# Kernel optimization log

Hardware: AMD Instinct MI355X
Metric: run time of the kernel (lower is better)

## Reference

```python
import jax, jax.numpy as jnp
import numpy as np

H = 768
NH = 12
HD = H // NH
FF = 3072
EPS = 1e-12
SCALE = 1.0 / (HD ** 0.5)


def _ln(x, g, b):
    m = jnp.mean(x, axis=-1, keepdims=True)
    v = jnp.mean((x - m) ** 2, axis=-1, keepdims=True)
    return (x - m) * jax.lax.rsqrt(v + EPS) * g + b


def setup_inputs() -> dict:
    key = jax.random.key(0)
    ks = jax.random.split(key, 16)
    B, Q, S, T = 8, 64, 48, 128
    s = 0.02
    return {
        "q": jax.random.normal(ks[0], (B, Q, H), jnp.float32),
        "k": jax.random.normal(ks[1], (B, S, T, H), jnp.float32),
        "mask": jax.random.randint(ks[2], (B, S, T), 0, 2, jnp.int32),
        "Wq": jax.random.normal(ks[3], (H, H), jnp.float32) * s,
        "Wkv": jax.random.normal(ks[4], (H, H), jnp.float32) * s,
        "Wo": jax.random.normal(ks[5], (H, H), jnp.float32) * s,
        "bo": jnp.zeros((H,), jnp.float32),
        "ln1_g": jnp.ones((H,), jnp.float32),
        "ln1_b": jnp.zeros((H,), jnp.float32),
        "W1": jax.random.normal(ks[6], (H, FF), jnp.float32) * s,
        "b1": jnp.zeros((FF,), jnp.float32),
        "W2": jax.random.normal(ks[7], (FF, H), jnp.float32) * s,
        "b2": jnp.zeros((H,), jnp.float32),
        "ln2_g": jnp.ones((H,), jnp.float32),
        "ln2_b": jnp.zeros((H,), jnp.float32),
    }


def reference(q, k, mask, Wq, Wkv, Wo, bo, ln1_g, ln1_b, W1, b1, W2, b2, ln2_g, ln2_b):
    B, Q, _ = q.shape
    _, S, T, _ = k.shape
    # projections (no bias)
    qp = (q @ Wq).reshape(B, Q, NH, HD)            # [b,q,h,d]
    kv = (k @ Wkv).reshape(B, S, T, NH, HD)        # [b,s,t,h,d]
    # broadcast-query grouped attention: softmax only over token dim t
    scores = jnp.einsum('bqhd,bsthd->bhqst', qp, kv) * SCALE
    scores = scores + mask.astype(scores.dtype)[:, None, None, :, :] * -10000.0
    alpha = jax.nn.softmax(scores, axis=-1)        # dropout is identity in eval
    res = jnp.einsum('bhqst,bsthd->bqshd', alpha, kv).reshape(B, Q, S, H)
    # BertSelfOutput with zero residual (residual=False)
    attn_out = _ln(res @ Wo + bo, ln1_g, ln1_b)    # [b,q,s,H]
    # FFN
    ffn = jax.nn.gelu(attn_out @ W1 + b1, approximate=False) @ W2 + b2
    return _ln(attn_out + ffn, ln2_g, ln2_b)
```

## Files before the change

### kernel.cpp

```cpp
#include <hip/hip_runtime.h>
#include <hip/hip_bf16.h>
#include <math.h>

#define B_ 8
#define Q_ 64
#define S_ 48
#define T_ 128
#define H_ 768
#define NH_ 12
#define HD_ 64
#define FF_ 3072

typedef float f32x4 __attribute__((ext_vector_type(4)));
typedef short s16x8 __attribute__((ext_vector_type(8)));
typedef short s16x4 __attribute__((ext_vector_type(4)));

__device__ __forceinline__ float ldT(const float* p, size_t i) { return p[i]; }
__device__ __forceinline__ float ldT(const __hip_bfloat16* p, size_t i) { return __bfloat162float(p[i]); }
__device__ __forceinline__ void stT(float* p, size_t i, float v) { p[i] = v; }
__device__ __forceinline__ void stT(__hip_bfloat16* p, size_t i, float v) { p[i] = __float2bfloat16(v); }

__device__ __forceinline__ short f2bf(float f) {
  __hip_bfloat16 h = __float2bfloat16(f);
  return *reinterpret_cast<short*>(&h);
}

__device__ __forceinline__ float gelu_f(float x) {
  float z = 1.5957691216f * (x + 0.044715f * x * x * x);
  z = fminf(z, 80.0f);
  float e = __expf(z);
  return x * e / (e + 1.0f);
}

__device__ __forceinline__ void gld_lds16(const void* g, void* l) {
  __builtin_amdgcn_global_load_lds(
      (const __attribute__((address_space(1))) void*)g,
      (__attribute__((address_space(3))) void*)l, 16, 0, 0);
}

__device__ __forceinline__ int swz_off(int row, int kc) {
  return row * 64 + ((kc ^ ((row >> 1) & 3)) << 4);
}

#define WAITV4() asm volatile("s_waitcnt vmcnt(4)" ::: "memory")
#define WAITV5() asm volatile("s_waitcnt vmcnt(5)" ::: "memory")
#define WAITV0() asm volatile("s_waitcnt vmcnt(0)" ::: "memory")
#define BARX()   do { __builtin_amdgcn_s_barrier(); asm volatile("" ::: "memory"); } while (0)

template<int KK, typename OT, bool BIAS, bool GELU>
__global__ __launch_bounds__(256) void gemm_mfma(
    const __hip_bfloat16* __restrict__ A,
    const __hip_bfloat16* __restrict__ BT,
    const float* __restrict__ bias, OT* __restrict__ C,
    int N, int nbx, int GB)
{
  constexpr int NT = KK / 32;
  static_assert(NT % 3 == 0 && NT >= 6, "KK must be multiple of 96");
  __shared__ char sm[3][16384];

  const int cpx = gridDim.x >> 3;
  const int xcd = blockIdx.x & 7;
  const int ci  = blockIdx.x >> 3;
  const int gsz = GB * nbx;
  const int g   = ci / gsz;
  const int r2  = ci - g * gsz;
  const int bn  = r2 / GB;
  const int bi  = r2 - bn * GB;
  const int bm  = xcd * (cpx / nbx) + g * GB + bi;
  const int m0 = bm * 128, n0 = bn * 128;

  const int tid = threadIdx.x;
  const int lane = tid & 63;
  const int wid = tid >> 6;
  const int wr = wid >> 1, wc = wid & 1;
  const int kcg = lane >> 4, rl = lane & 15;

  const __hip_bfloat16* pA[2];
  const __hip_bfloat16* pB[2];
  #pragma unroll
  for (int r = 0; r < 2; ++r) {
    const int c = tid + r * 256, row = c >> 2, slot = c & 3;
    const int kc = slot ^ ((row >> 1) & 3);
    pA[r] = A + (size_t)(m0 + row) * KK + kc * 8;
    pB[r] = BT + (size_t)(n0 + row) * KK + kc * 8;
  }
  auto stageT = [&](char* base, int off) {
    gld_lds16(pA[0] + off, base + tid * 16);
    gld_lds16(pA[1] + off, base + tid * 16 + 4096);
    gld_lds16(pB[0] + off, base + 8192 + tid * 16);
    gld_lds16(pB[1] + off, base + 8192 + tid * 16 + 4096);
  };

  int woffA[4], woffB[4];
  #pragma unroll
  for (int m = 0; m < 4; ++m)
    woffA[m] = swz_off(wr * 64 + m * 16 + rl, kcg);
  #pragma unroll
  for (int n = 0; n < 4; ++n)
    woffB[n] = 8192 + swz_off(wc * 64 + n * 16 + rl, kcg);

  f32x4 acc[4][4] = {};
  s16x8 af[4], bf[4];
  auto reads = [&](const char* base) {
    #pragma unroll
    for (int m = 0; m < 4; ++m) af[m] = *(const s16x8*)(base + woffA[m]);
    #pragma unroll
    for (int n = 0; n < 4; ++n) bf[n] = *(const s16x8*)(base + woffB[n]);
  };
  auto mfmas = [&]() {
    #pragma unroll
    for (int m = 0; m < 4; ++m)
      #pragma unroll
      for (int n = 0; n < 4; ++n)
        acc[m][n] = __builtin_amdgcn_mfma_f32_16x16x32_bf16(af[m], bf[n], acc[m][n], 0, 0, 0);
  };

  stageT(sm[0], 0);
  stageT(sm[1], 32);
  #pragma unroll
  for (int r = 0; r < 2; ++r) { pA[r] += 64; pB[r] += 64; }

  #pragma unroll 1
  for (int it = 0; it < NT / 3 - 1; ++it) {
    WAITV4(); BARX(); reads(sm[0]); stageT(sm[2], 0);  mfmas();
    WAITV4(); BARX(); reads(sm[1]); stageT(sm[0], 32); mfmas();
    WAITV4(); BARX(); reads(sm[2]); stageT(sm[1], 64); mfmas();
    #pragma unroll
    for (int r = 0; r < 2; ++r) { pA[r] += 96; pB[r] += 96; }
  }
  WAITV4(); BARX(); reads(sm[0]); stageT(sm[2], 0); mfmas();
  WAITV4(); BARX(); reads(sm[1]); mfmas();
  WAITV0(); BARX(); reads(sm[2]); mfmas();

  const int colb = n0 + wc * 64 + rl;
  const int rowb = m0 + wr * 64 + (lane >> 4) * 4;
  float bv[4];
  #pragma unroll
  for (int n = 0; n < 4; ++n) bv[n] = BIAS ? bias[colb + n * 16] : 0.0f;
  #pragma unroll
  for (int m = 0; m < 4; ++m) {
    #pragma unroll
    for (int r = 0; r < 4; ++r) {
      const int row = rowb + m * 16 + r;
      #pragma unroll
      for (int n = 0; n < 4; ++n) {
        float v = acc[m][n][r] + bv[n];
        if (GELU) v = gelu_f(v);
        stT(C, (size_t)row * N + colb + n * 16, v);
      }
    }
  }
}

template<int KK, typename OT, bool BIAS, bool GELU>
__global__ __launch_bounds__(256, 2) void gemm_fat(
    const __hip_bfloat16* __restrict__ A,
    const __hip_bfloat16* __restrict__ BT,
    const float* __restrict__ bias, OT* __restrict__ C,
    int N, int nbx, int GB)
{
  constexpr int NT = KK / 32;
  static_assert(NT % 3 == 0 && NT >= 6, "KK must be multiple of 96");
  __shared__ char sm[3][20480];

  const int cpx = gridDim.x >> 3;
  const int xcd = blockIdx.x & 7;
  const int ci  = blockIdx.x >> 3;
  const int gsz = GB * nbx;
  const int g   = ci / gsz;
  const int r2  = ci - g * gsz;
  const int bn  = r2 / GB;
  const int bi  = r2 - bn * GB;
  const int bm  = xcd * (cpx / nbx) + g * GB + bi;
  const int m0 = bm * 128, n0 = bn * 192;

  const int tid = threadIdx.x;
  const int lane = tid & 63;
  const int wid = tid >> 6;
  const int wm = wid >> 1;
  const int wn = wid & 1;
  const int kcg = lane >> 4, rl = lane & 15;

  const __hip_bfloat16* pA[2];
  const __hip_bfloat16* pB[3];
  #pragma unroll
  for (int r = 0; r < 2; ++r) {
    const int c = tid + r * 256, row = c >> 2, slot = c & 3;
    const int kc = slot ^ ((row >> 1) & 3);
    pA[r] = A + (size_t)(m0 + row) * KK + kc * 8;
  }
  #pragma unroll
  for (int r = 0; r < 3; ++r) {
    const int c = tid + r * 256, row = c >> 2, slot = c & 3;
    const int kc = slot ^ ((row >> 1) & 3);
    pB[r] = BT + (size_t)(n0 + row) * KK + kc * 8;
  }
  auto stageT = [&](char* base, int off) {
    gld_lds16(pA[0] + off, base + tid * 16);
    gld_lds16(pA[1] + off, base + tid * 16 + 4096);
    gld_lds16(pB[0] + off, base + 8192 + tid * 16);
    gld_lds16(pB[1] + off, base + 8192 + tid * 16 + 4096);
    gld_lds16(pB[2] + off, base + 8192 + tid * 16 + 8192);
  };

  int woffA[4], woffB[6];
  #pragma unroll
  for (int m = 0; m < 4; ++m)
    woffA[m] = swz_off(wm * 64 + m * 16 + rl, kcg);
  #pragma unroll
  for (int n = 0; n < 6; ++n)
    woffB[n] = 8192 + swz_off(wn * 96 + n * 16 + rl, kcg);

  f32x4 acc[4][6] = {};
  s16x8 af[4], bf[6];
  auto reads = [&](const char* base) {
    #pragma unroll
    for (int m = 0; m < 4; ++m) af[m] = *(const s16x8*)(base + woffA[m]);
    #pragma unroll
    for (int n = 0; n < 6; ++n) bf[n] = *(const s16x8*)(base + woffB[n]);
  };
  auto mfmas = [&]() {
    #pragma unroll
    for (int m = 0; m < 4; ++m)
      #pragma unroll
      for (int n = 0; n < 6; ++n)
        acc[m][n] = __builtin_amdgcn_mfma_f32_16x16x32_bf16(af[m], bf[n], acc[m][n], 0, 0, 0);
  };

  stageT(sm[0], 0);
  stageT(sm[1], 32);
  #pragma unroll
  for (int r = 0; r < 2; ++r) pA[r] += 64;
  #pragma unroll
  for (int r = 0; r < 3; ++r) pB[r] += 64;

  #pragma unroll 1
  for (int it = 0; it < NT / 3 - 1; ++it) {
    WAITV5(); BARX(); reads(sm[0]); stageT(sm[2], 0);  mfmas();
    WAITV5(); BARX(); reads(sm[1]); stageT(sm[0], 32); mfmas();
    WAITV5(); BARX(); reads(sm[2]); stageT(sm[1], 64); mfmas();
    #pragma unroll
    for (int r = 0; r < 2; ++r) pA[r] += 96;
    #pragma unroll
    for (int r = 0; r < 3; ++r) pB[r] += 96;
  }
  WAITV5(); BARX(); reads(sm[0]); stageT(sm[2], 0); mfmas();
  WAITV5(); BARX(); reads(sm[1]); mfmas();
  WAITV0(); BARX(); reads(sm[2]); mfmas();

  const int colb = n0 + wn * 96 + rl;
  const int rowb = m0 + wm * 64 + (lane >> 4) * 4;
  float bv[6];
  #pragma unroll
  for (int n = 0; n < 6; ++n) bv[n] = BIAS ? bias[colb + n * 16] : 0.0f;
  #pragma unroll
  for (int m = 0; m < 4; ++m) {
    #pragma unroll
    for (int r = 0; r < 4; ++r) {
      const int row = rowb + m * 16 + r;
      #pragma unroll
      for (int n = 0; n < 6; ++n) {
        float v = acc[m][n][r] + bv[n];
        if (GELU) v = gelu_f(v);
        stT(C, (size_t)row * N + colb + n * 16, v);
      }
    }
  }
}

template<typename OT>
__global__ __launch_bounds__(256) void gemm64(
    const float* __restrict__ A, const float* __restrict__ W,
    OT* __restrict__ C, int M, int N, int K)
{
  __shared__ float As[16][65];
  __shared__ float Ws[16][65];
  const int tid = threadIdx.x;
  const int m0 = blockIdx.y * 64;
  const int n0 = blockIdx.x * 64;
  const int tx = (tid & 15) * 4;
  const int ty = (tid >> 4) * 4;
  float acc[4][4] = {};

  for (int k0 = 0; k0 < K; k0 += 16) {
    #pragma unroll
    for (int r = 0; r < 4; ++r) {
      int idx = tid + r * 256;
      int mm = idx >> 4, kk = idx & 15;
      As[kk][mm] = A[(size_t)(m0 + mm) * K + (k0 + kk)];
    }
    #pragma unroll
    for (int r = 0; r < 4; ++r) {
      int idx = tid + r * 256;
      int kk = idx >> 6, nn = idx & 63;
      Ws[kk][nn] = W[(size_t)(k0 + kk) * N + (n0 + nn)];
    }
    __syncthreads();
    #pragma unroll
    for (int kk = 0; kk < 16; ++kk) {
      float a[4], b[4];
      #pragma unroll
      for (int i = 0; i < 4; ++i) a[i] = As[kk][ty + i];
      #pragma unroll
      for (int j = 0; j < 4; ++j) b[j] = Ws[kk][tx + j];
      #pragma unroll
      for (int i = 0; i < 4; ++i)
        #pragma unroll
        for (int j = 0; j < 4; ++j) acc[i][j] += a[i] * b[j];
    }
    __syncthreads();
  }
  #pragma unroll
  for (int i = 0; i < 4; ++i)
    #pragma unroll
    for (int j = 0; j < 4; ++j)
      stT(C, (size_t)(m0 + ty + i) * N + (n0 + tx + j), acc[i][j]);
}

__device__ __forceinline__ void tcast_body(
    const float* W, __hip_bfloat16* WT, int K, int N, int bx, int by, int tid,
    float (*t)[33])
{
  const int n0 = bx * 32, k0 = by * 32;
  const int x = tid & 31, y4 = (tid >> 5) * 4;
  #pragma unroll
  for (int i = 0; i < 4; ++i)
    t[y4 + i][x] = W[(size_t)(k0 + y4 + i) * N + n0 + x];
  __syncthreads();
  #pragma unroll
  for (int i = 0; i < 4; ++i)
    WT[(size_t)(n0 + y4 + i) * K + k0 + x] = __float2bfloat16(t[x][y4 + i]);
}

__global__ __launch_bounds__(256) void wtrans_all(
    const float* __restrict__ Wkv, __hip_bfloat16* __restrict__ WkvT,
    const float* __restrict__ Wo, __hip_bfloat16* __restrict__ WoT,
    const float* __restrict__ W1, __hip_bfloat16* __restrict__ W1T,
    const float* __restrict__ W2, __hip_bfloat16* __restrict__ W2T)
{
  __shared__ float t[32][33];
  const int bid = blockIdx.x;
  const int tid = threadIdx.x;
  if (bid < 576) {
    tcast_body(Wkv, WkvT, H_, H_, bid % 24, bid / 24, tid, t);
  } else if (bid < 1152) {
    const int s = bid - 576;
    tcast_body(Wo, WoT, H_, H_, s % 24, s / 24, tid, t);
  } else if (bid < 3456) {
    const int s = bid - 1152;
    tcast_body(W1, W1T, H_, FF_, s % 96, s / 96, tid, t);
  } else {
    const int s = bid - 3456;
    tcast_body(W2, W2T, FF_, H_, s % 24, s / 24, tid, t);
  }
}

__global__ __launch_bounds__(256) void cast_f32_bf16(
    const float* __restrict__ x, __hip_bfloat16* __restrict__ y, size_t n4)
{
  const size_t i = (size_t)blockIdx.x * 256 + threadIdx.x;
  if (i >= n4) return;
  const float4 v = ((const float4*)x)[i];
  __hip_bfloat16 o[4] = { __float2bfloat16(v.x), __float2bfloat16(v.y),
                          __float2bfloat16(v.z), __float2bfloat16(v.w) };
  *(ushort4*)(y + i * 4) = *(ushort4*)o;
}

__global__ __launch_bounds__(256) void attn_mfma(
    const __hip_bfloat16* __restrict__ qp,
    const __hip_bfloat16* __restrict__ kvp,
    const int* __restrict__ mask,
    __hip_bfloat16* __restrict__ res)
{
  const int s = blockIdx.x, h = blockIdx.y, b = blockIdx.z;
  __shared__ __align__(16) char lds[66048];
  char* Ks = lds;
  char* VT = lds + 16384;
  char* SC = lds + 32768;
  float* mv = (float*)(lds + 65536);

  const int tid = threadIdx.x;
  const int lane = tid & 63;
  const int wid = tid >> 6;
  const int wr = wid >> 1, wc = wid & 1;
  const int kcg = lane >> 4, rl = lane & 15;

  if (tid < 128) mv[tid] = (float)mask[((size_t)b * S_ + s) * T_ + tid] * -10000.0f;

  {
    const __hip_bfloat16* qb = qp + ((size_t)b * Q_) * H_ + h * HD_;
    #pragma unroll
    for (int r = 0; r < 2; ++r) {
      const int c = tid + r * 256;
      const int qq = c >> 3, sc = c & 7;
      const int kc8 = sc ^ (qq & 7);
      gld_lds16(qb + (size_t)qq * H_ + kc8 * 8, SC + c * 16);
    }
  }
  {
    const int kc8 = tid & 7, tg = tid >> 3;
    const int t0 = tg * 4;
    const __hip_bfloat16* kb = kvp + (((size_t)b * S_ + s) * T_) * H_ + h * HD_ + kc8 * 8;
    s16x8 r0 = *(const s16x8*)(kb + (size_t)(t0 + 0) * H_);
    s16x8 r1 = *(const s16x8*)(kb + (size_t)(t0 + 1) * H_);
    s16x8 r2 = *(const s16x8*)(kb + (size_t)(t0 + 2) * H_);
    s16x8 r3 = *(const s16x8*)(kb + (size_t)(t0 + 3) * H_);
    *(s16x8*)(Ks + (t0 + 0) * 128 + ((kc8 ^ ((t0 + 0) & 7)) << 4)) = r0;
    *(s16x8*)(Ks + (t0 + 1) * 128 + ((kc8 ^ ((t0 + 1) & 7)) << 4)) = r1;
    *(s16x8*)(Ks + (t0 + 2) * 128 + ((kc8 ^ ((t0 + 2) & 7)) << 4)) = r2;
    *(s16x8*)(Ks + (t0 + 3) * 128 + ((kc8 ^ ((t0 + 3) & 7)) << 4)) = r3;
    const int tc = tg >> 1;
    const int toff = (tg & 1) * 8;
    #pragma unroll
    for (int j = 0; j < 8; ++j) {
      s16x4 v4 = { r0[j], r1[j], r2[j], r3[j] };
      const int d = kc8 * 8 + j;
      *(s16x4*)(VT + d * 256 + ((tc ^ (d & 15)) << 4) + toff) = v4;
    }
  }
  __syncthreads();

  f32x4 acc[2][4] = {};
  {
    s16x8 af[2][2], bf[2][4];
    #pragma unroll
    for (int kk = 0; kk < 2; ++kk) {
      #pragma unroll
      for (int m = 0; m < 2; ++m) {
        const int q = wr * 32 + m * 16 + rl;
        const int kc8 = kk * 4 + kcg;
        af[kk][m] = *(const s16x8*)(SC + q * 128 + ((kc8 ^ (q & 7)) << 4));
      }
      #pragma unroll
      for (int n = 0; n < 4; ++n) {
        const int t = wc * 64 + n * 16 + rl;
        const int kc8 = kk * 4 + kcg;
        bf[kk][n] = *(const s16x8*)(Ks + t * 128 + ((kc8 ^ (t & 7)) << 4));
      }
    }
    #pragma unroll
    for (int kk = 0; kk < 2; ++kk)
      #pragma unroll
      for (int m = 0; m < 2; ++m)
        #pragma unroll
        for (int n = 0; n < 4; ++n)
          acc[m][n] = __builtin_amdgcn_mfma_f32_16x16x32_bf16(af[kk][m], bf[kk][n], acc[m][n], 0, 0, 0);
  }
  __syncthreads();

  #pragma unroll
  for (int m = 0; m < 2; ++m)
    #pragma unroll
    for (int n = 0; n < 4; ++n)
      #pragma unroll
      for (int r = 0; r < 4; ++r) {
        const int q = wr * 32 + m * 16 + (lane >> 4) * 4 + r;
        const int t = wc * 64 + n * 16 + rl;
        const int tc32 = t >> 2;
        *(float*)(SC + q * 512 + ((tc32 ^ (q & 31)) << 4) + (t & 3) * 4) =
            acc[m][n][r] * 0.125f + mv[t];
      }
  __syncthreads();

  {
    const int q = tid >> 2, quarter = tid & 3;
    float vals[32];
    #pragma unroll
    for (int j = 0; j < 8; ++j) {
      const int tc32 = quarter * 8 + j;
      const f32x4 c = *(const f32x4*)(SC + q * 512 + ((tc32 ^ (q & 31)) << 4));
      vals[j * 4 + 0] = c[0]; vals[j * 4 + 1] = c[1];
      vals[j * 4 + 2] = c[2]; vals[j * 4 + 3] = c[3];
    }
    float mx = -1e30f;
    #pragma unroll
    for (int i = 0; i < 32; ++i) mx = fmaxf(mx, vals[i]);
    mx = fmaxf(mx, __shfl_xor(mx, 1, 64));
    mx = fmaxf(mx, __shfl_xor(mx, 2, 64));
    float sum = 0.0f;
    #pragma unroll
    for (int i = 0; i < 32; ++i) { vals[i] = expf(vals[i] - mx); sum += vals[i]; }
    sum += __shfl_xor(sum, 1, 64);
    sum += __shfl_xor(sum, 2, 64);
    const float inv = 1.0f / sum;
    #pragma unroll
    for (int jj = 0; jj < 4; ++jj) {
      const int tcp = quarter * 4 + jj;
      s16x8 pk;
      #pragma unroll
      for (int i = 0; i < 8; ++i) pk[i] = f2bf(vals[jj * 8 + i] * inv);
      *(s16x8*)(SC + q * 512 + ((tcp ^ (q & 15)) << 4)) = pk;
    }
  }
  __syncthreads();

  f32x4 oacc[2][2] = {};
  #pragma unroll
  for (int kt = 0; kt < 4; ++kt) {
    s16x8 pa[2], vb[2];
    #pragma unroll
    for (int m = 0; m < 2; ++m) {
      const int q = wr * 32 + m * 16 + rl;
      const int tcp = kt * 4 + kcg;
      pa[m] = *(const s16x8*)(SC + q * 512 + ((tcp ^ (q & 15)) << 4));
    }
    #pragma unroll
    for (int n = 0; n < 2; ++n) {
      const int d = wc * 32 + n * 16 + rl;
      const int tc = kt * 4 + kcg;
      vb[n] = *(const s16x8*)(VT + d * 256 + ((tc ^ (d & 15)) << 4));
    }
    #pragma unroll
    for (int m = 0; m < 2; ++m)
      #pragma unroll
      for (int n = 0; n < 2; ++n)
        oacc[m][n] = __builtin_amdgcn_mfma_f32_16x16x32_bf16(pa[m], vb[n], oacc[m][n], 0, 0, 0);
  }
  #pragma unroll
  for (int m = 0; m < 2; ++m)
    #pragma unroll
    for (int n = 0; n < 2; ++n)
      #pragma unroll
      for (int r = 0; r < 4; ++r) {
        const int q = wr * 32 + m * 16 + (lane >> 4) * 4 + r;
        const int d = wc * 32 + n * 16 + rl;
        res[(((size_t)b * Q_ + q) * S_ + s) * H_ + h * HD_ + d] =
            __float2bfloat16(oacc[m][n][r]);
      }
}

template<bool ADD, typename IT, typename OT>
__global__ __launch_bounds__(256) void ln_kernel(
    const IT* __restrict__ X, const IT* __restrict__ X2,
    const float* __restrict__ g, const float* __restrict__ bta,
    OT* __restrict__ Y)
{
  const size_t row = blockIdx.x;
  const int tid = threadIdx.x;
  float v[3];
  #pragma unroll
  for (int i = 0; i < 3; ++i) {
    int c = tid + i * 256;
    v[i] = ldT(X, row * H_ + c);
    if (ADD) v[i] += ldT(X2, row * H_ + c);
  }
  float sum = v[0] + v[1] + v[2];
  #pragma unroll
  for (int off = 32; off > 0; off >>= 1) sum += __shfl_down(sum, off, 64);
  __shared__ float red[8];
  const int w = tid >> 6;
  if ((tid & 63) == 0) red[w] = sum;
  __syncthreads();
  const float mean = (red[0] + red[1] + red[2] + red[3]) * (1.0f / 768.0f);
  float vs = 0.0f;
  #pragma unroll
  for (int i = 0; i < 3; ++i) { v[i] -= mean; vs += v[i] * v[i]; }
  #pragma unroll
  for (int off = 32; off > 0; off >>= 1) vs += __shfl_down(vs, off, 64);
  if ((tid & 63) == 0) red[4 + w] = vs;
  __syncthreads();
  const float rstd = rsqrtf((red[4] + red[5] + red[6] + red[7]) * (1.0f / 768.0f) + 1e-12f);
  #pragma unroll
  for (int i = 0; i < 3; ++i) {
    int c = tid + i * 256;
    stT(Y, row * H_ + c, v[i] * rstd * g[c] + bta[c]);
  }
}

extern "C" void kernel_launch(void* const* d_in, const int* in_sizes, int n_in,
                              void* d_out, int out_size, void* d_ws, size_t ws_size,
                              hipStream_t stream) {
  const float* q    = (const float*)d_in[0];
  const float* k    = (const float*)d_in[1];
  const int*   mask = (const int*)d_in[2];
  const float* Wq   = (const float*)d_in[3];
  const float* Wkv  = (const float*)d_in[4];
  const float* Wo   = (const float*)d_in[5];
  const float* bo   = (const float*)d_in[6];
  const float* ln1g = (const float*)d_in[7];
  const float* ln1b = (const float*)d_in[8];
  const float* W1   = (const float*)d_in[9];
  const float* b1   = (const float*)d_in[10];
  const float* W2   = (const float*)d_in[11];
  const float* b2   = (const float*)d_in[12];
  const float* ln2g = (const float*)d_in[13];
  const float* ln2b = (const float*)d_in[14];
  float* out = (float*)d_out;

  const int MROWS = B_ * Q_ * S_;
  const int KVROWS = B_ * S_ * T_;

  char* ws = (char*)d_ws;
  __hip_bfloat16* kbf  = (__hip_bfloat16*)ws;
  __hip_bfloat16* apre = (__hip_bfloat16*)ws;
  __hip_bfloat16* kvp  = (__hip_bfloat16*)(ws + 75497472);
  __hip_bfloat16* ffn1 = (__hip_bfloat16*)ws;
  __hip_bfloat16* ares = (__hip_bfloat16*)(ws + 150994944);
  __hip_bfloat16* ffn2 = ares;
  __hip_bfloat16* aln  = (__hip_bfloat16*)(ws + 188743680);
  __hip_bfloat16* qp   = (__hip_bfloat16*)(ws + 226492416);
  __hip_bfloat16* WkvT = (__hip_bfloat16*)(ws + 228065280);
  __hip_bfloat16* WoT  = (__hip_bfloat16*)(ws + 229244928);
  __hip_bfloat16* W1T  = (__hip_bfloat16*)(ws + 230424576);
  __hip_bfloat16* W2T  = (__hip_bfloat16*)(ws + 235143168);

  dim3 blk(256);

  cast_f32_bf16<<<dim3((KVROWS * H_ / 4 + 255) / 256), blk, 0, stream>>>(
      k, kbf, (size_t)KVROWS * H_ / 4);
  wtrans_all<<<dim3(5760), blk, 0, stream>>>(
      Wkv, WkvT, Wo, WoT, W1, W1T, W2, W2T);

  gemm64<__hip_bfloat16><<<dim3(H_ / 64, 512 / 64), blk, 0, stream>>>(
      q, Wq, qp, 512, H_, H_);
  gemm_mfma<768, __hip_bfloat16, false, false>
      <<<dim3((KVROWS / 128) * (H_ / 128)), blk, 0, stream>>>(
      kbf, WkvT, nullptr, kvp, H_, H_ / 128, 6);
  attn_mfma<<<dim3(S_, NH_, B_), blk, 0, stream>>>(qp, kvp, mask, ares);
  gemm_mfma<768, __hip_bfloat16, true, false>
      <<<dim3((MROWS / 128) * (H_ / 128)), blk, 0, stream>>>(
      ares, WoT, bo, apre, H_, H_ / 128, 6);
  ln_kernel<false, __hip_bfloat16, __hip_bfloat16><<<MROWS, blk, 0, stream>>>(
      apre, nullptr, ln1g, ln1b, aln);
  gemm_fat<768, __hip_bfloat16, true, true>
      <<<dim3((MROWS / 128) * (FF_ / 192)), blk, 0, stream>>>(
      aln, W1T, b1, ffn1, FF_, FF_ / 192, 6);
  gemm_fat<3072, __hip_bfloat16, true, false>
      <<<dim3((MROWS / 128) * (H_ / 192)), blk, 0, stream>>>(
      ffn1, W2T, b2, ffn2, H_, H_ / 192, 6);
  ln_kernel<true, __hip_bfloat16, float><<<MROWS, blk, 0, stream>>>(
      aln, ffn2, ln2g, ln2b, out);
}
```

Measured before the change: 581.0 us.

## Split-K the Wo and W2 GEMMs and fold the partial sums into LayerNorm

Adds a SPLIT template parameter to both MFMA GEMM kernels. The K dimension is divided in two across twice as many blocks, and each half writes its partial result to a separate bf16 buffer. The LayerNorm kernel now sums the partial buffers (and the residual) while it loads them, so no separate reduction kernel is needed. The aim is more blocks for the under-filled Wo and W2 GEMMs (W2 had only 768 blocks with K=3072). The cost is extra partial-output traffic, an extra bf16 rounding of each partial sum, and shorter K loops per block.

```diff
diff --git a/kernel.cpp b/kernel.cpp
--- a/kernel.cpp
+++ b/kernel.cpp
@@ -47,20 +47,26 @@
 #define WAITV0() asm volatile("s_waitcnt vmcnt(0)" ::: "memory")
 #define BARX()   do { __builtin_amdgcn_s_barrier(); asm volatile("" ::: "memory"); } while (0)
 
-template<int KK, typename OT, bool BIAS, bool GELU>
+template<int KK, int SPLIT, typename OT, bool BIAS, bool GELU>
 __global__ __launch_bounds__(256) void gemm_mfma(
     const __hip_bfloat16* __restrict__ A,
     const __hip_bfloat16* __restrict__ BT,
-    const float* __restrict__ bias, OT* __restrict__ C,
+    const float* __restrict__ bias, OT* __restrict__ C, OT* __restrict__ C2,
     int N, int nbx, int GB)
 {
-  constexpr int NT = KK / 32;
-  static_assert(NT % 3 == 0 && NT >= 6, "KK must be multiple of 96");
+  constexpr int KH = KK / SPLIT;
+  constexpr int NT = KH / 32;
+  static_assert(NT % 3 == 0 && NT >= 6, "KH must be multiple of 96");
   __shared__ char sm[3][16384];
 
-  const int cpx = gridDim.x >> 3;
-  const int xcd = blockIdx.x & 7;
-  const int ci  = blockIdx.x >> 3;
+  int bid = blockIdx.x, spl = 0;
+  if (SPLIT == 2) {
+    const int hf = gridDim.x >> 1;
+    if (bid >= hf) { spl = 1; bid -= hf; }
+  }
+  const int cpx = (SPLIT == 2 ? (gridDim.x >> 1) : gridDim.x) >> 3;
+  const int xcd = bid & 7;
+  const int ci  = bid >> 3;
   const int gsz = GB * nbx;
   const int g   = ci / gsz;
   const int r2  = ci - g * gsz;
@@ -68,6 +74,8 @@
   const int bi  = r2 - bn * GB;
   const int bm  = xcd * (cpx / nbx) + g * GB + bi;
   const int m0 = bm * 128, n0 = bn * 128;
+  const int k00 = spl * KH;
+  OT* Cw = spl ? C2 : C;
 
   const int tid = threadIdx.x;
   const int lane = tid & 63;
@@ -81,8 +89,8 @@
   for (int r = 0; r < 2; ++r) {
     const int c = tid + r * 256, row = c >> 2, slot = c & 3;
     const int kc = slot ^ ((row >> 1) & 3);
-    pA[r] = A + (size_t)(m0 + row) * KK + kc * 8;
-    pB[r] = BT + (size_t)(n0 + row) * KK + kc * 8;
+    pA[r] = A + (size_t)(m0 + row) * KK + k00 + kc * 8;
+    pB[r] = BT + (size_t)(n0 + row) * KK + k00 + kc * 8;
   }
   auto stageT = [&](char* base, int off) {
     gld_lds16(pA[0] + off, base + tid * 16);
@@ -136,7 +144,8 @@
   const int rowb = m0 + wr * 64 + (lane >> 4) * 4;
   float bv[4];
   #pragma unroll
-  for (int n = 0; n < 4; ++n) bv[n] = BIAS ? bias[colb + n * 16] : 0.0f;
+  for (int n = 0; n < 4; ++n)
+    bv[n] = (BIAS && spl == 0) ? bias[colb + n * 16] : 0.0f;
   #pragma unroll
   for (int m = 0; m < 4; ++m) {
     #pragma unroll
@@ -146,26 +155,32 @@
       for (int n = 0; n < 4; ++n) {
         float v = acc[m][n][r] + bv[n];
         if (GELU) v = gelu_f(v);
-        stT(C, (size_t)row * N + colb + n * 16, v);
+        stT(Cw, (size_t)row * N + colb + n * 16, v);
       }
     }
   }
 }
 
-template<int KK, typename OT, bool BIAS, bool GELU>
+template<int KK, int SPLIT, typename OT, bool BIAS, bool GELU>
 __global__ __launch_bounds__(256, 2) void gemm_fat(
     const __hip_bfloat16* __restrict__ A,
     const __hip_bfloat16* __restrict__ BT,
-    const float* __restrict__ bias, OT* __restrict__ C,
+    const float* __restrict__ bias, OT* __restrict__ C, OT* __restrict__ C2,
     int N, int nbx, int GB)
 {
-  constexpr int NT = KK / 32;
-  static_assert(NT % 3 == 0 && NT >= 6, "KK must be multiple of 96");
+  constexpr int KH = KK / SPLIT;
+  constexpr int NT = KH / 32;
+  static_assert(NT % 3 == 0 && NT >= 6, "KH must be multiple of 96");
   __shared__ char sm[3][20480];
 
-  const int cpx = gridDim.x >> 3;
-  const int xcd = blockIdx.x & 7;
-  const int ci  = blockIdx.x >> 3;
+  int bid = blockIdx.x, spl = 0;
+  if (SPLIT == 2) {
+    const int hf = gridDim.x >> 1;
+    if (bid >= hf) { spl = 1; bid -= hf; }
+  }
+  const int cpx = (SPLIT == 2 ? (gridDim.x >> 1) : gridDim.x) >> 3;
+  const int xcd = bid & 7;
+  const int ci  = bid >> 3;
   const int gsz = GB * nbx;
   const int g   = ci / gsz;
   const int r2  = ci - g * gsz;
@@ -173,6 +188,8 @@
   const int bi  = r2 - bn * GB;
   const int bm  = xcd * (cpx / nbx) + g * GB + bi;
   const int m0 = bm * 128, n0 = bn * 192;
+  const int k00 = spl * KH;
+  OT* Cw = spl ? C2 : C;
 
   const int tid = threadIdx.x;
   const int lane = tid & 63;
@@ -187,13 +204,13 @@
   for (int r = 0; r < 2; ++r) {
     const int c = tid + r * 256, row = c >> 2, slot = c & 3;
     const int kc = slot ^ ((row >> 1) & 3);
-    pA[r] = A + (size_t)(m0 + row) * KK + kc * 8;
+    pA[r] = A + (size_t)(m0 + row) * KK + k00 + kc * 8;
   }
   #pragma unroll
   for (int r = 0; r < 3; ++r) {
     const int c = tid + r * 256, row = c >> 2, slot = c & 3;
     const int kc = slot ^ ((row >> 1) & 3);
-    pB[r] = BT + (size_t)(n0 + row) * KK + kc * 8;
+    pB[r] = BT + (size_t)(n0 + row) * KK + k00 + kc * 8;
   }
   auto stageT = [&](char* base, int off) {
     gld_lds16(pA[0] + off, base + tid * 16);
@@ -252,7 +269,8 @@
   const int rowb = m0 + wm * 64 + (lane >> 4) * 4;
   float bv[6];
   #pragma unroll
-  for (int n = 0; n < 6; ++n) bv[n] = BIAS ? bias[colb + n * 16] : 0.0f;
+  for (int n = 0; n < 6; ++n)
+    bv[n] = (BIAS && spl == 0) ? bias[colb + n * 16] : 0.0f;
   #pragma unroll
   for (int m = 0; m < 4; ++m) {
     #pragma unroll
@@ -262,7 +280,7 @@
       for (int n = 0; n < 6; ++n) {
         float v = acc[m][n][r] + bv[n];
         if (GELU) v = gelu_f(v);
-        stT(C, (size_t)row * N + colb + n * 16, v);
+        stT(Cw, (size_t)row * N + colb + n * 16, v);
       }
     }
   }
@@ -529,9 +547,10 @@
       }
 }
 
-template<bool ADD, typename IT, typename OT>
+template<int NADD, typename IT, typename OT>
 __global__ __launch_bounds__(256) void ln_kernel(
     const IT* __restrict__ X, const IT* __restrict__ X2,
+    const IT* __restrict__ X3,
     const float* __restrict__ g, const float* __restrict__ bta,
     OT* __restrict__ Y)
 {
@@ -542,7 +561,8 @@
   for (int i = 0; i < 3; ++i) {
     int c = tid + i * 256;
     v[i] = ldT(X, row * H_ + c);
-    if (ADD) v[i] += ldT(X2, row * H_ + c);
+    if (NADD >= 1) v[i] += ldT(X2, row * H_ + c);
+    if (NADD >= 2) v[i] += ldT(X3, row * H_ + c);
   }
   float sum = v[0] + v[1] + v[2];
   #pragma unroll
@@ -591,18 +611,20 @@
   const int KVROWS = B_ * S_ * T_;
 
   char* ws = (char*)d_ws;
-  __hip_bfloat16* kbf  = (__hip_bfloat16*)ws;
-  __hip_bfloat16* apre = (__hip_bfloat16*)ws;
-  __hip_bfloat16* kvp  = (__hip_bfloat16*)(ws + 75497472);
-  __hip_bfloat16* ffn1 = (__hip_bfloat16*)ws;
-  __hip_bfloat16* ares = (__hip_bfloat16*)(ws + 150994944);
-  __hip_bfloat16* ffn2 = ares;
-  __hip_bfloat16* aln  = (__hip_bfloat16*)(ws + 188743680);
-  __hip_bfloat16* qp   = (__hip_bfloat16*)(ws + 226492416);
-  __hip_bfloat16* WkvT = (__hip_bfloat16*)(ws + 228065280);
-  __hip_bfloat16* WoT  = (__hip_bfloat16*)(ws + 229244928);
-  __hip_bfloat16* W1T  = (__hip_bfloat16*)(ws + 230424576);
-  __hip_bfloat16* W2T  = (__hip_bfloat16*)(ws + 235143168);
+  __hip_bfloat16* kbf   = (__hip_bfloat16*)ws;
+  __hip_bfloat16* aprea = (__hip_bfloat16*)ws;
+  __hip_bfloat16* apreb = (__hip_bfloat16*)(ws + 37748736);
+  __hip_bfloat16* kvp   = (__hip_bfloat16*)(ws + 75497472);
+  __hip_bfloat16* ffn1  = (__hip_bfloat16*)ws;
+  __hip_bfloat16* ares  = (__hip_bfloat16*)(ws + 150994944);
+  __hip_bfloat16* ffn2a = ares;
+  __hip_bfloat16* aln   = (__hip_bfloat16*)(ws + 188743680);
+  __hip_bfloat16* qp    = (__hip_bfloat16*)(ws + 226492416);
+  __hip_bfloat16* WkvT  = (__hip_bfloat16*)(ws + 228065280);
+  __hip_bfloat16* WoT   = (__hip_bfloat16*)(ws + 229244928);
+  __hip_bfloat16* W1T   = (__hip_bfloat16*)(ws + 230424576);
+  __hip_bfloat16* W2T   = (__hip_bfloat16*)(ws + 235143168);
+  __hip_bfloat16* ffn2b = (__hip_bfloat16*)(ws + 239861760);
 
   dim3 blk(256);
 
@@ -613,21 +635,21 @@
 
   gemm64<__hip_bfloat16><<<dim3(H_ / 64, 512 / 64), blk, 0, stream>>>(
       q, Wq, qp, 512, H_, H_);
-  gemm_mfma<768, __hip_bfloat16, false, false>
+  gemm_mfma<768, 1, __hip_bfloat16, false, false>
       <<<dim3((KVROWS / 128) * (H_ / 128)), blk, 0, stream>>>(
-      kbf, WkvT, nullptr, kvp, H_, H_ / 128, 6);
+      kbf, WkvT, nullptr, kvp, nullptr, H_, H_ / 128, 6);
   attn_mfma<<<dim3(S_, NH_, B_), blk, 0, stream>>>(qp, kvp, mask, ares);
-  gemm_mfma<768, __hip_bfloat16, true, false>
-      <<<dim3((MROWS / 128) * (H_ / 128)), blk, 0, stream>>>(
-      ares, WoT, bo, apre, H_, H_ / 128, 6);
-  ln_kernel<false, __hip_bfloat16, __hip_bfloat16><<<MROWS, blk, 0, stream>>>(
-      apre, nullptr, ln1g, ln1b, aln);
-  gemm_fat<768, __hip_bfloat16, true, true>
+  gemm_mfma<768, 2, __hip_bfloat16, true, false>
+      <<<dim3(2 * (MROWS / 128) * (H_ / 128)), blk, 0, stream>>>(
+      ares, WoT, bo, aprea, apreb, H_, H_ / 128, 6);
+  ln_kernel<1, __hip_bfloat16, __hip_bfloat16><<<MROWS, blk, 0, stream>>>(
+      aprea, apreb, nullptr, ln1g, ln1b, aln);
+  gemm_fat<768, 1, __hip_bfloat16, true, true>
       <<<dim3((MROWS / 128) * (FF_ / 192)), blk, 0, stream>>>(
-      aln, W1T, b1, ffn1, FF_, FF_ / 192, 6);
-  gemm_fat<3072, __hip_bfloat16, true, false>
-      <<<dim3((MROWS / 128) * (H_ / 192)), blk, 0, stream>>>(
-      ffn1, W2T, b2, ffn2, H_, H_ / 192, 6);
-  ln_kernel<true, __hip_bfloat16, float><<<MROWS, blk, 0, stream>>>(
-      aln, ffn2, ln2g, ln2b, out);
-}
+      aln, W1T, b1, ffn1, nullptr, FF_, FF_ / 192, 6);
+  gemm_fat<3072, 2, __hip_bfloat16, true, false>
+      <<<dim3(2 * (MROWS / 128) * (H_ / 192)), blk, 0, stream>>>(
+      ffn1, W2T, b2, ffn2a, ffn2b, H_, H_ / 192, 6);
+  ln_kernel<2, __hip_bfloat16, float><<<MROWS, blk, 0, stream>>>(
+      aln, ffn2a, ffn2b, ln2g, ln2b, out);
+}
```

Result: slower. 603.4 us (+3.9%).
